# Performance work log

Hardware: AMD Instinct MI355X
Metric: run time of the kernel (lower is better)

## Reference

```python
import jax, jax.numpy as jnp
import numpy as np

CHUNK_FRAMES = 100
LOOKAHEAD_FRAMES = 50
NUM_HEADS = 16


def _allowed_mask(T):
    # frame i attends to j iff chunk(j) <= chunk(i) OR j <= i + lookahead
    pos = jnp.arange(T)
    chunk = pos // CHUNK_FRAMES
    chunk_ok = chunk[None, :] <= chunk[:, None]          # (T, T) keys per query row
    look_ok = pos[None, :] <= pos[:, None] + LOOKAHEAD_FRAMES
    return chunk_ok | look_ok                             # bool (T, T)


def setup_inputs() -> dict:
    key = jax.random.key(0)
    ks = jax.random.split(key, 8)
    B, T, D = 4, 1500, 1024
    s = 1.0 / np.sqrt(D)
    return {
        "hidden_states": jax.random.normal(ks[0], (B, T, D), jnp.float32),
        "Wq": jax.random.normal(ks[1], (D, D), jnp.float32) * s,
        "bq": jax.random.normal(ks[2], (D,), jnp.float32) * 0.02,
        "Wk": jax.random.normal(ks[3], (D, D), jnp.float32) * s,
        "Wv": jax.random.normal(ks[4], (D, D), jnp.float32) * s,
        "bv": jax.random.normal(ks[5], (D,), jnp.float32) * 0.02,
        "Wo": jax.random.normal(ks[6], (D, D), jnp.float32) * s,
        "bo": jax.random.normal(ks[7], (D,), jnp.float32) * 0.02,
    }


def reference(hidden_states, Wq, bq, Wk, Wv, bv, Wo, bo):
    B, T, D = hidden_states.shape
    H = NUM_HEADS
    hd = D // H
    scale = hd ** -0.5

    # Whisper attention: q scaled, k_proj has no bias
    q = (hidden_states @ Wq + bq) * scale       # (B, T, D)
    k = hidden_states @ Wk                       # (B, T, D)
    v = hidden_states @ Wv + bv                  # (B, T, D)

    q = q.reshape(B, T, H, hd)
    k = k.reshape(B, T, H, hd)
    v = v.reshape(B, T, H, hd)

    scores = jnp.einsum("bqhd,bkhd->bhqk", q, k)  # (B, H, T, T)
    allowed = _allowed_mask(T)                     # (T, T)
    neg = jnp.asarray(jnp.finfo(scores.dtype).min, scores.dtype)
    scores = jnp.where(allowed[None, None, :, :], scores, neg)

    attn = jax.nn.softmax(scores, axis=-1)
    out = jnp.einsum("bhqk,bkhd->bqhd", attn, v).reshape(B, T, D)
    return out @ Wo + bo
```

## Files before the change

kernel.cpp:

```cpp
#include <hip/hip_runtime.h>
#include <hip/hip_bf16.h>


typedef unsigned short u16;
typedef unsigned int   u32;
typedef unsigned long long u64;
typedef __attribute__((ext_vector_type(8))) short bf16x8;
typedef __attribute__((ext_vector_type(4))) float f32x4;

typedef const __attribute__((address_space(1))) u32 gu32;
typedef __attribute__((address_space(3))) u32 lu32;

__device__ __forceinline__ void load_lds16(void* lds, const void* g) {
    __builtin_amdgcn_global_load_lds((gu32*)g, (lu32*)lds, 16, 0, 0);
}

__device__ __forceinline__ u16 f2bf(float x) {
    u32 u = __builtin_bit_cast(u32, x);
    u = (u + 0x7fffu + ((u >> 16) & 1u)) >> 16;
    return (u16)u;
}

__device__ __forceinline__ u32 pkbf(float a, float b) {
    __hip_bfloat162 t = __float22bfloat162_rn(float2{a, b});
    u32 r;
    __builtin_memcpy(&r, &t, 4);
    return r;
}

__device__ __forceinline__ float fexp2(float x) {
#if __has_builtin(__builtin_amdgcn_exp2f)
    return __builtin_amdgcn_exp2f(x);
#else
    return exp2f(x);
#endif
}

#define NTOK 6000
#define QSCALE 0.18033688011112042f

__global__ __launch_bounds__(256) void wa_cvt_x(const float* __restrict__ X,
                                                u16* __restrict__ Xb) {
    size_t i = ((size_t)blockIdx.x * 256 + threadIdx.x) * 4;
    if (i >= (size_t)6144000) return;
    float4 v = *(const float4*)(X + i);
    u64 p = (u64)f2bf(v.x) | ((u64)f2bf(v.y) << 16)
          | ((u64)f2bf(v.z) << 32) | ((u64)f2bf(v.w) << 48);
    *(u64*)(Xb + i) = p;
}

__global__ __launch_bounds__(256) void wa_pack_w(const float* __restrict__ Wq,
                                                 const float* __restrict__ Wk,
                                                 const float* __restrict__ Wv,
                                                 const float* __restrict__ Wo,
                                                 u16* __restrict__ Wt,
                                                 u16* __restrict__ Wto) {
    __shared__ float tile[64][65];
    const int n0 = blockIdx.x * 64;
    const int k0 = blockIdx.y * 64;
    const float* src; u16* dst; int cn;
    if (n0 < 3072) {
        int sel = n0 >> 10;
        src = (sel == 0) ? Wq : ((sel == 1) ? Wk : Wv);
        cn = n0 & 1023;
        dst = Wt + (size_t)n0 * 1024;
    } else {
        src = Wo; cn = n0 - 3072;
        dst = Wto + (size_t)(n0 - 3072) * 1024;
    }
    const int t = threadIdx.x;
    #pragma unroll
    for (int i = 0; i < 16; i++) {
        int idx = t + i * 256;
        int r = idx >> 6, c = idx & 63;
        tile[r][c] = src[(size_t)(k0 + r) * 1024 + cn + c];
    }
    __syncthreads();
    #pragma unroll
    for (int i = 0; i < 16; i++) {
        int idx = t + i * 256;
        int nr = idx >> 6, kc = idx & 63;
        dst[(size_t)nr * 1024 + k0 + kc] = f2bf(tile[kc][nr]);
    }
}

template<int EPI>
__global__ __launch_bounds__(256) void wa_gemm(
        const u16* __restrict__ A, const u16* __restrict__ Bt,
        const float* __restrict__ bq, const float* __restrict__ bv,
        u16* __restrict__ Qb, u16* __restrict__ Kb, u16* __restrict__ Vt,
        const float* __restrict__ bo, float* __restrict__ outF) {
    __shared__ u16 As[2][128 * 32];
    __shared__ u16 Bs[2][128 * 32];
    const int tid = threadIdx.x;
    const int wave = tid >> 6, lane = tid & 63;
    const int wm = wave >> 1, wn = wave & 1;
    const int r = lane & 15, g = lane >> 4;
    const int m0 = blockIdx.x * 128, n0 = blockIdx.y * 128;
    const bool swp = (EPI == 1) || (n0 < 2048);

    const f32x4 z4 = {0.f, 0.f, 0.f, 0.f};
    f32x4 acc[4][4];
    #pragma unroll
    for (int i = 0; i < 4; i++)
        #pragma unroll
        for (int j = 0; j < 4; j++)
            acc[i][j] = z4;

    const int srow = wave * 32 + (lane >> 2);
    const int scol = (lane & 3) * 8;
    const u16* aSrc = A + (size_t)(m0 + srow) * 1024 + scol;
    const u16* bSrc = Bt + (size_t)(n0 + srow) * 1024 + scol;

#define GSTAGE(K0, BUF) do {                                                  \
        load_lds16((char*)As[BUF] + wave * 2048,        aSrc + (K0));         \
        load_lds16((char*)As[BUF] + wave * 2048 + 1024, aSrc + 16 * 1024 + (K0)); \
        load_lds16((char*)Bs[BUF] + wave * 2048,        bSrc + (K0));         \
        load_lds16((char*)Bs[BUF] + wave * 2048 + 1024, bSrc + 16 * 1024 + (K0)); \
    } while (0)

    GSTAGE(0, 0);
    __syncthreads();
    int cur = 0;

    for (int k0 = 0; k0 < 1024; k0 += 32) {
        if (k0 + 32 < 1024) GSTAGE(k0 + 32, cur ^ 1);
        bf16x8 a[4], b[4];
        #pragma unroll
        for (int i = 0; i < 4; i++)
            a[i] = *(const bf16x8*)&As[cur][(wm * 64 + i * 16 + r) * 32 + g * 8];
        #pragma unroll
        for (int j = 0; j < 4; j++)
            b[j] = *(const bf16x8*)&Bs[cur][(wn * 64 + j * 16 + r) * 32 + g * 8];
        if (swp) {
            #pragma unroll
            for (int i = 0; i < 4; i++)
                #pragma unroll
                for (int j = 0; j < 4; j++)
                    acc[i][j] = __builtin_amdgcn_mfma_f32_16x16x32_bf16(b[j], a[i], acc[i][j], 0, 0, 0);
        } else {
            #pragma unroll
            for (int i = 0; i < 4; i++)
                #pragma unroll
                for (int j = 0; j < 4; j++)
                    acc[i][j] = __builtin_amdgcn_mfma_f32_16x16x32_bf16(a[i], b[j], acc[i][j], 0, 0, 0);
        }
        __syncthreads();
        cur ^= 1;
    }
#undef GSTAGE

    if constexpr (EPI == 0) {
        const int sel = n0 >> 10;
        if (sel < 2) {
            #pragma unroll
            for (int i = 0; i < 4; i++) {
                int gm = m0 + wm * 64 + i * 16 + r;
                if (gm >= NTOK) continue;
                int bb = gm / 1500, tt = gm - bb * 1500;
                #pragma unroll
                for (int j = 0; j < 4; j++) {
                    int w0 = (n0 & 1023) + wn * 64 + j * 16 + g * 4;
                    int h = w0 >> 6, d0 = w0 & 63;
                    u16* dst = (sel == 0 ? Qb : Kb)
                             + ((size_t)(bb * 16 + h) * 1500 + tt) * 64 + d0;
                    u64 pk;
                    if (sel == 0) {
                        float4 bqv = *(const float4*)(bq + w0);
                        pk = (u64)f2bf((acc[i][j][0] + bqv.x) * QSCALE)
                           | ((u64)f2bf((acc[i][j][1] + bqv.y) * QSCALE) << 16)
                           | ((u64)f2bf((acc[i][j][2] + bqv.z) * QSCALE) << 32)
                           | ((u64)f2bf((acc[i][j][3] + bqv.w) * QSCALE) << 48);
                    } else {
                        pk = (u64)f2bf(acc[i][j][0])
                           | ((u64)f2bf(acc[i][j][1]) << 16)
                           | ((u64)f2bf(acc[i][j][2]) << 32)
                           | ((u64)f2bf(acc[i][j][3]) << 48);
                    }
                    *(u64*)dst = pk;
                }
            }
        } else {
            #pragma unroll
            for (int j = 0; j < 4; j++) {
                int gn = n0 + wn * 64 + j * 16 + r;
                int w = gn & 1023;
                int h = w >> 6, d = w & 63;
                float bias = bv[w];
                #pragma unroll
                for (int i = 0; i < 4; i++) {
                    int gm0 = m0 + wm * 64 + i * 16 + g * 4;
                    if (gm0 >= NTOK) continue;
                    int bb = gm0 / 1500, tt0 = gm0 - bb * 1500;
                    u64 pk = (u64)f2bf(acc[i][j][0] + bias)
                           | ((u64)f2bf(acc[i][j][1] + bias) << 16)
                           | ((u64)f2bf(acc[i][j][2] + bias) << 32)
                           | ((u64)f2bf(acc[i][j][3] + bias) << 48);
                    *(u64*)(Vt + ((size_t)(bb * 16 + h) * 64 + d) * 1504 + tt0) = pk;
                }
            }
        }
    } else {
        #pragma unroll
        for (int i = 0; i < 4; i++) {
            int gm = m0 + wm * 64 + i * 16 + r;
            if (gm >= NTOK) continue;
            #pragma unroll
            for (int j = 0; j < 4; j++) {
                int gn0 = n0 + wn * 64 + j * 16 + g * 4;
                float4 bov = *(const float4*)(bo + gn0);
                float4 v = {acc[i][j][0] + bov.x, acc[i][j][1] + bov.y,
                            acc[i][j][2] + bov.z, acc[i][j][3] + bov.w};
                *(float4*)(outF + (size_t)gm * 1024 + gn0) = v;
            }
        }
    }
}

__global__ __launch_bounds__(256) void wa_attn(const u16* __restrict__ Qb,
                                               const u16* __restrict__ Kb,
                                               const u16* __restrict__ Vt,
                                               u16* __restrict__ Ob) {
    __shared__ u16 Ks[2][64 * 64];
    __shared__ u16 Vs[2][64 * 64];
    __shared__ u16 Ps[4][16 * 64];
    const int tid = threadIdx.x, wave = tid >> 6, lane = tid & 63;
    const int q = lane & 15, g = lane >> 4;
    const int bid = blockIdx.x;
    const int qt = (bid >> 3) % 24;
    const int plane = ((bid >> 3) / 24) * 8 + (bid & 7);
    const int h = plane & 15, b = plane >> 4;

    const int qr = qt * 64 + wave * 16 + q;
    const int qc = qr < 1500 ? qr : 1499;
    int Lq = (qr / 100 + 1) * 100;
    { int la = qr + 51; if (la > Lq) Lq = la; }
    if (Lq > 1500) Lq = 1500;
    int qmax = qt * 64 + 63; if (qmax > 1499) qmax = 1499;
    int Lb = (qmax / 100 + 1) * 100;
    { int lb2 = qmax + 51; if (lb2 > Lb) Lb = lb2; }
    if (Lb > 1500) Lb = 1500;
    const int ntiles = (Lb + 63) >> 6;

    const u16* qp = Qb + ((size_t)plane * 1500 + qc) * 64 + g * 8;
    const bf16x8 qa0 = *(const bf16x8*)qp;
    const bf16x8 qa1 = *(const bf16x8*)(qp + 32);

    const f32x4 z4 = {0.f, 0.f, 0.f, 0.f};
    f32x4 accO[4];
    #pragma unroll
    for (int dt = 0; dt < 4; dt++) accO[dt] = z4;
    float m_run = -3.0e38f, l_run = 0.f;

    const int sRow = wave * 16 + (lane >> 3);
    const int sO = (lane & 7) * 16;
    const u16* kBase = Kb + (size_t)plane * 1500 * 64;
    const u16* vBase = Vt + (size_t)plane * 64 * 1504;

#define STAGE(J0, BUF) do {                                              \
        _Pragma("unroll")                                                \
        for (int i_ = 0; i_ < 2; i_++) {                                 \
            int row_ = sRow + i_ * 8;                                    \
            int so_ = sO ^ ((row_ & 7) << 4);                            \
            int key_ = (J0) + row_; if (key_ > 1499) key_ = 1499;        \
            load_lds16((char*)Ks[BUF] + wave * 2048 + i_ * 1024,         \
                       kBase + (size_t)key_ * 64 + (so_ >> 1));          \
            int vc_ = (J0) + (so_ >> 1); if (vc_ > 1496) vc_ = 1496;     \
            load_lds16((char*)Vs[BUF] + wave * 2048 + i_ * 1024,         \
                       vBase + (size_t)row_ * 1504 + vc_);               \
        } } while (0)

    STAGE(0, 0);
    __syncthreads();
    int cur = 0;

    for (int ti = 0; ti < ntiles; ti++) {
        const int j0 = ti << 6;
        if (ti + 1 < ntiles) STAGE(j0 + 64, cur ^ 1);

        const char* kb = (const char*)Ks[cur];
        const char* vb = (const char*)Vs[cur];

        f32x4 st[4];
        #pragma unroll
        for (int t = 0; t < 4; t++) {
            f32x4 s = z4;
            #pragma unroll
            for (int ks = 0; ks < 2; ks++) {
                int krow = t * 16 + q;
                int cb = (ks * 64 + g * 16) ^ ((krow & 7) << 4);
                bf16x8 kf = *(const bf16x8*)(kb + krow * 128 + cb);
                s = __builtin_amdgcn_mfma_f32_16x16x32_bf16(kf, ks ? qa1 : qa0, s, 0, 0, 0);
            }
            st[t] = s;
        }

        float p[16];
        float mt = -3.0e38f;
        #pragma unroll
        for (int t = 0; t < 4; t++)
            #pragma unroll
            for (int e = 0; e < 4; e++) {
                int key = j0 + t * 16 + g * 4 + e;
                float sv = (key < Lq) ? st[t][e] : -3.0e38f;
                p[t * 4 + e] = sv;
                mt = fmaxf(mt, sv);
            }
        mt = fmaxf(mt, __shfl_xor(mt, 16));
        mt = fmaxf(mt, __shfl_xor(mt, 32));
        float m_new = fmaxf(m_run, mt);
        float resc = fexp2(m_run - m_new);
        float sum = 0.f;
        #pragma unroll
        for (int i = 0; i < 16; i++) { p[i] = fexp2(p[i] - m_new); sum += p[i]; }
        sum += __shfl_xor(sum, 16);
        sum += __shfl_xor(sum, 32);
        l_run = l_run * resc + sum;
        m_run = m_new;
        #pragma unroll
        for (int dt = 0; dt < 4; dt++) accO[dt] *= resc;

        {
            char* pw = (char*)Ps[wave];
            const int sw = (q & 7) << 4;
            #pragma unroll
            for (int t = 0; t < 4; t++) {
                u32 lo = pkbf(p[t * 4 + 0], p[t * 4 + 1]);
                u32 hi = pkbf(p[t * 4 + 2], p[t * 4 + 3]);
                int c0 = t * 32 + g * 8;
                *(u32*)(pw + q * 128 + ((c0)     ^ sw)) = lo;
                *(u32*)(pw + q * 128 + ((c0 + 4) ^ sw)) = hi;
            }
        }
        asm volatile("" ::: "memory");

        #pragma unroll
        for (int s2 = 0; s2 < 2; s2++) {
            int cb = s2 * 64 + g * 16;
            bf16x8 pf = *(const bf16x8*)((const char*)Ps[wave] + q * 128 + (cb ^ ((q & 7) << 4)));
            #pragma unroll
            for (int dt = 0; dt < 4; dt++) {
                int dr = dt * 16 + q;
                bf16x8 vf = *(const bf16x8*)(vb + dr * 128 + (cb ^ ((dr & 7) << 4)));
                accO[dt] = __builtin_amdgcn_mfma_f32_16x16x32_bf16(vf, pf, accO[dt], 0, 0, 0);
            }
        }

        __syncthreads();
        cur ^= 1;
    }
#undef STAGE

    float inv = 1.0f / l_run;
    if (qr < 1500) {
        u16* op = Ob + ((size_t)(b * 1500 + qr)) * 1024 + h * 64 + g * 4;
        #pragma unroll
        for (int dt = 0; dt < 4; dt++) {
            u32 lo = pkbf(accO[dt][0] * inv, accO[dt][1] * inv);
            u32 hi = pkbf(accO[dt][2] * inv, accO[dt][3] * inv);
            *(u64*)(op + dt * 16) = (u64)lo | ((u64)hi << 32);
        }
    }
}

extern "C" void kernel_launch(void* const* d_in, const int* in_sizes, int n_in,
                              void* d_out, int out_size, void* d_ws, size_t ws_size,
                              hipStream_t stream) {
    (void)in_sizes; (void)n_in; (void)out_size; (void)ws_size;
    const float* X  = (const float*)d_in[0];
    const float* Wq = (const float*)d_in[1];
    const float* bq = (const float*)d_in[2];
    const float* Wk = (const float*)d_in[3];
    const float* Wv = (const float*)d_in[4];
    const float* bv = (const float*)d_in[5];
    const float* Wo = (const float*)d_in[6];
    const float* bo = (const float*)d_in[7];
    float* out = (float*)d_out;

    u16* Xb  = (u16*)d_ws;
    u16* Wt  = Xb  + (size_t)6016 * 1024;
    u16* Wto = Wt  + (size_t)3072 * 1024;
    u16* Qb  = Wto + (size_t)1024 * 1024;
    u16* Kb  = Qb  + (size_t)64 * 1500 * 64;
    u16* Vt  = Kb  + (size_t)64 * 1500 * 64;

    wa_cvt_x<<<6000, 256, 0, stream>>>(X, Xb);
    wa_pack_w<<<dim3(64, 16), 256, 0, stream>>>(Wq, Wk, Wv, Wo, Wt, Wto);
    wa_gemm<0><<<dim3(47, 24), 256, 0, stream>>>(Xb, Wt, bq, bv, Qb, Kb, Vt, nullptr, nullptr);
    wa_attn<<<1536, 256, 0, stream>>>(Qb, Kb, Vt, Xb);
    wa_gemm<1><<<dim3(47, 8), 256, 0, stream>>>(Xb, Wto, nullptr, nullptr, nullptr, nullptr, nullptr, bo, out);
}
```

Baseline: 191.0 us.

## Use 256x256 tiles with 8 waves for QKV projection GEMM

```diff
diff --git a/kernel.cpp b/kernel.cpp
--- a/kernel.cpp
+++ b/kernel.cpp
@@ -84,11 +84,123 @@
     }
 }
 
-template<int EPI>
-__global__ __launch_bounds__(256) void wa_gemm(
+__global__ __launch_bounds__(512) void wa_gemm0(
         const u16* __restrict__ A, const u16* __restrict__ Bt,
         const float* __restrict__ bq, const float* __restrict__ bv,
-        u16* __restrict__ Qb, u16* __restrict__ Kb, u16* __restrict__ Vt,
+        u16* __restrict__ Qb, u16* __restrict__ Kb, u16* __restrict__ Vt) {
+    __shared__ u16 As[2][256 * 32];
+    __shared__ u16 Bs[2][256 * 32];
+    const int tid = threadIdx.x;
+    const int wave = tid >> 6, lane = tid & 63;
+    const int wm = wave >> 2, wn = wave & 3;
+    const int r = lane & 15, g = lane >> 4;
+    const int m0 = blockIdx.x * 256, n0 = blockIdx.y * 256;
+    const bool swp = (n0 < 2048);
+
+    const f32x4 z4 = {0.f, 0.f, 0.f, 0.f};
+    f32x4 acc[8][4];
+    #pragma unroll
+    for (int i = 0; i < 8; i++)
+        #pragma unroll
+        for (int j = 0; j < 4; j++)
+            acc[i][j] = z4;
+
+    const int srow = wave * 32 + (lane >> 2);
+    const int scol = (lane & 3) * 8;
+    const u16* aSrc = A + (size_t)(m0 + srow) * 1024 + scol;
+    const u16* bSrc = Bt + (size_t)(n0 + srow) * 1024 + scol;
+
+#define GSTAGE(K0, BUF) do {                                                  \
+        load_lds16((char*)As[BUF] + wave * 2048,        aSrc + (K0));         \
+        load_lds16((char*)As[BUF] + wave * 2048 + 1024, aSrc + 16 * 1024 + (K0)); \
+        load_lds16((char*)Bs[BUF] + wave * 2048,        bSrc + (K0));         \
+        load_lds16((char*)Bs[BUF] + wave * 2048 + 1024, bSrc + 16 * 1024 + (K0)); \
+    } while (0)
+
+    GSTAGE(0, 0);
+    __syncthreads();
+    int cur = 0;
+
+    for (int k0 = 0; k0 < 1024; k0 += 32) {
+        if (k0 + 32 < 1024) GSTAGE(k0 + 32, cur ^ 1);
+        bf16x8 a[8], b[4];
+        #pragma unroll
+        for (int i = 0; i < 8; i++)
+            a[i] = *(const bf16x8*)&As[cur][(wm * 128 + i * 16 + r) * 32 + g * 8];
+        #pragma unroll
+        for (int j = 0; j < 4; j++)
+            b[j] = *(const bf16x8*)&Bs[cur][(wn * 64 + j * 16 + r) * 32 + g * 8];
+        if (swp) {
+            #pragma unroll
+            for (int i = 0; i < 8; i++)
+                #pragma unroll
+                for (int j = 0; j < 4; j++)
+                    acc[i][j] = __builtin_amdgcn_mfma_f32_16x16x32_bf16(b[j], a[i], acc[i][j], 0, 0, 0);
+        } else {
+            #pragma unroll
+            for (int i = 0; i < 8; i++)
+                #pragma unroll
+                for (int j = 0; j < 4; j++)
+                    acc[i][j] = __builtin_amdgcn_mfma_f32_16x16x32_bf16(a[i], b[j], acc[i][j], 0, 0, 0);
+        }
+        __syncthreads();
+        cur ^= 1;
+    }
+#undef GSTAGE
+
+    const int sel = n0 >> 10;
+    if (sel < 2) {
+        #pragma unroll
+        for (int i = 0; i < 8; i++) {
+            int gm = m0 + wm * 128 + i * 16 + r;
+            if (gm >= NTOK) continue;
+            int bb = gm / 1500, tt = gm - bb * 1500;
+            #pragma unroll
+            for (int j = 0; j < 4; j++) {
+                int w0 = (n0 & 1023) + wn * 64 + j * 16 + g * 4;
+                int h = w0 >> 6, d0 = w0 & 63;
+                u16* dst = (sel == 0 ? Qb : Kb)
+                         + ((size_t)(bb * 16 + h) * 1500 + tt) * 64 + d0;
+                u64 pk;
+                if (sel == 0) {
+                    float4 bqv = *(const float4*)(bq + w0);
+                    pk = (u64)f2bf((acc[i][j][0] + bqv.x) * QSCALE)
+                       | ((u64)f2bf((acc[i][j][1] + bqv.y) * QSCALE) << 16)
+                       | ((u64)f2bf((acc[i][j][2] + bqv.z) * QSCALE) << 32)
+                       | ((u64)f2bf((acc[i][j][3] + bqv.w) * QSCALE) << 48);
+                } else {
+                    pk = (u64)f2bf(acc[i][j][0])
+                       | ((u64)f2bf(acc[i][j][1]) << 16)
+                       | ((u64)f2bf(acc[i][j][2]) << 32)
+                       | ((u64)f2bf(acc[i][j][3]) << 48);
+                }
+                *(u64*)dst = pk;
+            }
+        }
+    } else {
+        #pragma unroll
+        for (int j = 0; j < 4; j++) {
+            int gn = n0 + wn * 64 + j * 16 + r;
+            int w = gn & 1023;
+            int h = w >> 6, d = w & 63;
+            float bias = bv[w];
+            #pragma unroll
+            for (int i = 0; i < 8; i++) {
+                int gm0 = m0 + wm * 128 + i * 16 + g * 4;
+                if (gm0 >= NTOK) continue;
+                int bb = gm0 / 1500, tt0 = gm0 - bb * 1500;
+                u64 pk = (u64)f2bf(acc[i][j][0] + bias)
+                       | ((u64)f2bf(acc[i][j][1] + bias) << 16)
+                       | ((u64)f2bf(acc[i][j][2] + bias) << 32)
+                       | ((u64)f2bf(acc[i][j][3] + bias) << 48);
+                *(u64*)(Vt + ((size_t)(bb * 16 + h) * 64 + d) * 1504 + tt0) = pk;
+            }
+        }
+    }
+}
+
+__global__ __launch_bounds__(256) void wa_gemm1(
+        const u16* __restrict__ A, const u16* __restrict__ Bt,
         const float* __restrict__ bo, float* __restrict__ outF) {
     __shared__ u16 As[2][128 * 32];
     __shared__ u16 Bs[2][128 * 32];
@@ -97,7 +209,6 @@
     const int wm = wave >> 1, wn = wave & 1;
     const int r = lane & 15, g = lane >> 4;
     const int m0 = blockIdx.x * 128, n0 = blockIdx.y * 128;
-    const bool swp = (EPI == 1) || (n0 < 2048);
 
     const f32x4 z4 = {0.f, 0.f, 0.f, 0.f};
     f32x4 acc[4][4];
@@ -132,87 +243,27 @@
         #pragma unroll
         for (int j = 0; j < 4; j++)
             b[j] = *(const bf16x8*)&Bs[cur][(wn * 64 + j * 16 + r) * 32 + g * 8];
-        if (swp) {
-            #pragma unroll
-            for (int i = 0; i < 4; i++)
-                #pragma unroll
-                for (int j = 0; j < 4; j++)
-                    acc[i][j] = __builtin_amdgcn_mfma_f32_16x16x32_bf16(b[j], a[i], acc[i][j], 0, 0, 0);
-        } else {
-            #pragma unroll
-            for (int i = 0; i < 4; i++)
-                #pragma unroll
-                for (int j = 0; j < 4; j++)
-                    acc[i][j] = __builtin_amdgcn_mfma_f32_16x16x32_bf16(a[i], b[j], acc[i][j], 0, 0, 0);
-        }
+        #pragma unroll
+        for (int i = 0; i < 4; i++)
+            #pragma unroll
+            for (int j = 0; j < 4; j++)
+                acc[i][j] = __builtin_amdgcn_mfma_f32_16x16x32_bf16(b[j], a[i], acc[i][j], 0, 0, 0);
         __syncthreads();
         cur ^= 1;
     }
 #undef GSTAGE
 
-    if constexpr (EPI == 0) {
-        const int sel = n0 >> 10;
-        if (sel < 2) {
-            #pragma unroll
-            for (int i = 0; i < 4; i++) {
-                int gm = m0 + wm * 64 + i * 16 + r;
-                if (gm >= NTOK) continue;
-                int bb = gm / 1500, tt = gm - bb * 1500;
-                #pragma unroll
-                for (int j = 0; j < 4; j++) {
-                    int w0 = (n0 & 1023) + wn * 64 + j * 16 + g * 4;
-                    int h = w0 >> 6, d0 = w0 & 63;
-                    u16* dst = (sel == 0 ? Qb : Kb)
-                             + ((size_t)(bb * 16 + h) * 1500 + tt) * 64 + d0;
-                    u64 pk;
-                    if (sel == 0) {
-                        float4 bqv = *(const float4*)(bq + w0);
-                        pk = (u64)f2bf((acc[i][j][0] + bqv.x) * QSCALE)
-                           | ((u64)f2bf((acc[i][j][1] + bqv.y) * QSCALE) << 16)
-                           | ((u64)f2bf((acc[i][j][2] + bqv.z) * QSCALE) << 32)
-                           | ((u64)f2bf((acc[i][j][3] + bqv.w) * QSCALE) << 48);
-                    } else {
-                        pk = (u64)f2bf(acc[i][j][0])
-                           | ((u64)f2bf(acc[i][j][1]) << 16)
-                           | ((u64)f2bf(acc[i][j][2]) << 32)
-                           | ((u64)f2bf(acc[i][j][3]) << 48);
-                    }
-                    *(u64*)dst = pk;
-                }
-            }
-        } else {
-            #pragma unroll
-            for (int j = 0; j < 4; j++) {
-                int gn = n0 + wn * 64 + j * 16 + r;
-                int w = gn & 1023;
-                int h = w >> 6, d = w & 63;
-                float bias = bv[w];
-                #pragma unroll
-                for (int i = 0; i < 4; i++) {
-                    int gm0 = m0 + wm * 64 + i * 16 + g * 4;
-                    if (gm0 >= NTOK) continue;
-                    int bb = gm0 / 1500, tt0 = gm0 - bb * 1500;
-                    u64 pk = (u64)f2bf(acc[i][j][0] + bias)
-                           | ((u64)f2bf(acc[i][j][1] + bias) << 16)
-                           | ((u64)f2bf(acc[i][j][2] + bias) << 32)
-                           | ((u64)f2bf(acc[i][j][3] + bias) << 48);
-                    *(u64*)(Vt + ((size_t)(bb * 16 + h) * 64 + d) * 1504 + tt0) = pk;
-                }
-            }
-        }
-    } else {
-        #pragma unroll
-        for (int i = 0; i < 4; i++) {
-            int gm = m0 + wm * 64 + i * 16 + r;
-            if (gm >= NTOK) continue;
-            #pragma unroll
-            for (int j = 0; j < 4; j++) {
-                int gn0 = n0 + wn * 64 + j * 16 + g * 4;
-                float4 bov = *(const float4*)(bo + gn0);
-                float4 v = {acc[i][j][0] + bov.x, acc[i][j][1] + bov.y,
-                            acc[i][j][2] + bov.z, acc[i][j][3] + bov.w};
-                *(float4*)(outF + (size_t)gm * 1024 + gn0) = v;
-            }
+    #pragma unroll
+    for (int i = 0; i < 4; i++) {
+        int gm = m0 + wm * 64 + i * 16 + r;
+        if (gm >= NTOK) continue;
+        #pragma unroll
+        for (int j = 0; j < 4; j++) {
+            int gn0 = n0 + wn * 64 + j * 16 + g * 4;
+            float4 bov = *(const float4*)(bo + gn0);
+            float4 v = {acc[i][j][0] + bov.x, acc[i][j][1] + bov.y,
+                        acc[i][j][2] + bov.z, acc[i][j][3] + bov.w};
+            *(float4*)(outF + (size_t)gm * 1024 + gn0) = v;
         }
     }
 }
@@ -386,7 +437,7 @@
 
     wa_cvt_x<<<6000, 256, 0, stream>>>(X, Xb);
     wa_pack_w<<<dim3(64, 16), 256, 0, stream>>>(Wq, Wk, Wv, Wo, Wt, Wto);
-    wa_gemm<0><<<dim3(47, 24), 256, 0, stream>>>(Xb, Wt, bq, bv, Qb, Kb, Vt, nullptr, nullptr);
+    wa_gemm0<<<dim3(24, 12), 512, 0, stream>>>(Xb, Wt, bq, bv, Qb, Kb, Vt);
     wa_attn<<<1536, 256, 0, stream>>>(Qb, Kb, Vt, Xb);
-    wa_gemm<1><<<dim3(47, 8), 256, 0, stream>>>(Xb, Wto, nullptr, nullptr, nullptr, nullptr, nullptr, bo, out);
-}
+    wa_gemm1<<<dim3(47, 8), 256, 0, stream>>>(Xb, Wto, bo, out);
+}
```

New measurement: 643.3 us. +236.8%, slower.
